# Kernel tuning notes

Hardware: AMD Instinct MI355X
Metric: run time of the kernel (lower is better)

The kernel has to match this reference:

```python
import jax, jax.numpy as jnp
import numpy as np

NB, NC = 100000, 10000   # buildings, communities
EB, EC = 400000, 80000   # edges
BD, CD = 64, 32          # feature dims


def _glorot(key, shape):
    fan_in = shape[-2] if len(shape) > 1 else shape[0]
    return jax.random.normal(key, shape, jnp.float32) * (1.0 / np.sqrt(fan_in))


def setup_inputs() -> dict:
    key = jax.random.key(0)
    ks = iter(jax.random.split(key, 40))
    inp = {}
    inp['building_features'] = jax.random.normal(next(ks), (NB, BD), jnp.float32)
    inp['community_features'] = jax.random.normal(next(ks), (NC, CD), jnp.float32)
    inp['building_edge_index'] = jax.random.randint(next(ks), (2, EB), 0, NB, jnp.int32)
    inp['community_edge_index'] = jax.random.randint(next(ks), (2, EC), 0, NC, jnp.int32)
    inp['building_to_comm_mapping'] = jax.random.randint(next(ks), (NB,), 0, NC, jnp.int32)
    inp['c1_wl'] = _glorot(next(ks), (CD, 512)); inp['c1_wr'] = _glorot(next(ks), (CD, 512))
    inp['c1_att'] = _glorot(next(ks), (8, 64)); inp['c1_b'] = jnp.zeros((512,), jnp.float32)
    inp['c2_wl'] = _glorot(next(ks), (512, 128)); inp['c2_wr'] = _glorot(next(ks), (512, 128))
    inp['c2_att'] = _glorot(next(ks), (4, 32)); inp['c2_b'] = jnp.zeros((128,), jnp.float32)
    # feature attention: 8 heads of MLP (64+128)->128->2
    inp['fa_w1'] = _glorot(next(ks), (8, BD + 128, 128)); inp['fa_b1'] = jnp.zeros((8, 128), jnp.float32)
    inp['fa_w2'] = _glorot(next(ks), (8, 128, 2)); inp['fa_b2'] = jnp.zeros((8, 2), jnp.float32)
    inp['b1_wl'] = _glorot(next(ks), (BD + 128, 512)); inp['b1_wr'] = _glorot(next(ks), (BD + 128, 512))
    inp['b1_att'] = _glorot(next(ks), (8, 64)); inp['b1_b'] = jnp.zeros((512,), jnp.float32)
    inp['b2_wl'] = _glorot(next(ks), (512, 128)); inp['b2_wr'] = _glorot(next(ks), (512, 128))
    inp['b2_att'] = _glorot(next(ks), (4, 32)); inp['b2_b'] = jnp.zeros((128,), jnp.float32)
    inp['b3_wl'] = _glorot(next(ks), (128, 2)); inp['b3_wr'] = _glorot(next(ks), (128, 2))
    inp['b3_att'] = _glorot(next(ks), (1, 2)); inp['b3_b'] = jnp.zeros((2,), jnp.float32)
    return inp


def gatv2(x, src, dst, wl, wr, att, b, heads, out_dim, concat=True):
    """PyG GATv2Conv (eval mode, self-loops already appended to src/dst)."""
    n = x.shape[0]
    xl = (x @ wl).reshape(n, heads, out_dim)  # source transform
    xr = (x @ wr).reshape(n, heads, out_dim)  # target transform
    e = jax.nn.leaky_relu(xl[src] + xr[dst], 0.2)          # [E,H,D]
    logits = jnp.einsum('ehd,hd->eh', e, att)              # [E,H]
    m = jax.ops.segment_max(logits, dst, num_segments=n)   # stable softmax per target
    p = jnp.exp(logits - m[dst])
    denom = jax.ops.segment_sum(p, dst, num_segments=n)
    alpha = p / denom[dst]
    agg = jax.ops.segment_sum(alpha[:, :, None] * xl[src], dst, num_segments=n)
    agg = agg.reshape(n, heads * out_dim) if concat else agg.mean(axis=1)
    return agg + b


def _with_self_loops(edge_index, n):
    loops = jnp.arange(n, dtype=edge_index.dtype)
    return (jnp.concatenate([edge_index[0], loops]), jnp.concatenate([edge_index[1], loops]))


def _forward(building_features, community_features,
             c1_wl, c1_wr, c1_att, c1_b, c2_wl, c2_wr, c2_att, c2_b,
             fa_w1, fa_b1, fa_w2, fa_b2,
             b1_wl, b1_wr, b1_att, b1_b, b2_wl, b2_wr, b2_att, b2_b,
             b3_wl, b3_wr, b3_att, b3_b,
             building_edge_index, community_edge_index, building_to_comm_mapping):
    csrc, cdst = _with_self_loops(community_edge_index, NC)
    bsrc, bdst = _with_self_loops(building_edge_index, NB)
    # community GNN (dropout is identity in eval)
    cx = jax.nn.relu(gatv2(community_features, csrc, cdst, c1_wl, c1_wr, c1_att, c1_b, 8, 64))
    cx = jax.nn.relu(gatv2(cx, csrc, cdst, c2_wl, c2_wr, c2_att, c2_b, 4, 32))  # [NC,128]
    bcf = cx[building_to_comm_mapping]                                          # [NB,128]
    # multi-head feature attention fusion (vectorized over 8 heads)
    combined = jnp.concatenate([building_features, bcf], axis=1)                # [NB,192]
    h = jax.nn.relu(jnp.einsum('nf,hfk->nhk', combined, fa_w1) + fa_b1)         # [NB,8,128]
    w = jax.nn.softmax(jnp.einsum('nhk,hko->nho', h, fa_w2) + fa_b2, axis=-1)   # [NB,8,2]
    wmean = w.mean(axis=1)                                                      # mean over heads == mean of weighted copies
    fused = jnp.concatenate([building_features * wmean[:, 0:1], bcf * wmean[:, 1:2]], axis=1)
    # building GNN (single batched graph == Batch.from_data_list over all communities)
    x = jax.nn.relu(gatv2(fused, bsrc, bdst, b1_wl, b1_wr, b1_att, b1_b, 8, 64))
    x = jax.nn.relu(gatv2(x, bsrc, bdst, b2_wl, b2_wr, b2_att, b2_b, 4, 32))
    x = gatv2(x, bsrc, bdst, b3_wl, b3_wr, b3_att, b3_b, 1, 2)                   # [NB,2]
    return jax.nn.log_softmax(x, axis=1)


def reference(building_features, community_features,
              c1_wl, c1_wr, c1_att, c1_b, c2_wl, c2_wr, c2_att, c2_b,
              fa_w1, fa_b1, fa_w2, fa_b2,
              b1_wl, b1_wr, b1_att, b1_b, b2_wl, b2_wr, b2_att, b2_b,
              b3_wl, b3_wr, b3_att, b3_b,
              building_edge_index, community_edge_index, building_to_comm_mapping):
    return _forward(building_features, community_features,
                    c1_wl, c1_wr, c1_att, c1_b, c2_wl, c2_wr, c2_att, c2_b,
                    fa_w1, fa_b1, fa_w2, fa_b2,
                    b1_wl, b1_wr, b1_att, b1_b, b2_wl, b2_wr, b2_att, b2_b,
                    b3_wl, b3_wr, b3_att, b3_b,
                    building_edge_index, community_edge_index, building_to_comm_mapping)
```

## Files before the change

### kernel.cpp

```cpp
#include <hip/hip_runtime.h>

static constexpr int NBLD = 100000, NCOM = 10000, EBU = 400000, ECO = 80000;
static constexpr int EBT = EBU + NBLD;
static constexpr int ECT = ECO + NCOM;

typedef _Float16 f16;
typedef _Float16 f16x2 __attribute__((ext_vector_type(2)));
typedef _Float16 f16x8 __attribute__((ext_vector_type(8)));
typedef float f32x4 __attribute__((ext_vector_type(4)));

static constexpr size_t OFF_X1H  = 0;
static constexpr size_t OFF_CXL  = 0;
static constexpr size_t OFF_CXR  = 20480000;
static constexpr size_t OFF_CX1  = 40960000;
static constexpr size_t OFF_CX2L = 61440000;
static constexpr size_t OFF_CX2R = 66560000;
static constexpr size_t OFF_X2   = 0;
static constexpr size_t OFF_XLH  = 102400000;
static constexpr size_t OFF_XRH  = 128000000;
static constexpr size_t OFF_XL2  = 102400000;
static constexpr size_t OFF_XR2  = 128000000;
static constexpr size_t OFF_BF16 = 153600000;
static constexpr size_t OFF_CXF16= 166400000;
static constexpr size_t OFF_WM   = 168960000;
static constexpr size_t OFF_XL3  = 169760000;
static constexpr size_t OFF_XR3  = 170560000;
static constexpr size_t OFF_FAW  = 171360000;
static constexpr size_t OFF_B1LT = 171753216;
static constexpr size_t OFF_B1RT = 171949824;
static constexpr size_t OFF_B2LT = 172146432;
static constexpr size_t OFF_B2RT = 172277504;
static constexpr size_t OFF_BOFF = 172408576;
static constexpr size_t OFF_BCUR = 172808592;
static constexpr size_t OFF_BSRC = 173208592;
static constexpr size_t OFF_COFF = 175208592;
static constexpr size_t OFF_CCUR = 175248608;
static constexpr size_t OFF_CSRC = 175288608;
static constexpr size_t OFF_SC1  = 175648608;
static constexpr size_t OFF_SC2  = 175649632;

__global__ void k_zero(int* __restrict__ p, int n) {
  int i = blockIdx.x * blockDim.x + threadIdx.x;
  if (i < n) p[i] = 0;
}

__global__ void k_zerof(float* __restrict__ p, int n) {
  int i = blockIdx.x * blockDim.x + threadIdx.x;
  if (i < n) p[i] = 0.f;
}

__global__ void k_cvt4(const float* __restrict__ a, f16* __restrict__ b, int n4) {
  int i = blockIdx.x * blockDim.x + threadIdx.x;
  if (i >= n4) return;
  float4 f = *(const float4*)(a + (size_t)i * 4);
  f16x2 h0; h0[0] = (f16)f.x; h0[1] = (f16)f.y;
  f16x2 h1; h1[0] = (f16)f.z; h1[1] = (f16)f.w;
  *(unsigned*)(b + (size_t)i * 4)     = __builtin_bit_cast(unsigned, h0);
  *(unsigned*)(b + (size_t)i * 4 + 2) = __builtin_bit_cast(unsigned, h1);
}

__global__ void k_cvtwb(const float* __restrict__ W, f16* __restrict__ WT, int K, int N) {
  int i = blockIdx.x * blockDim.x + threadIdx.x;
  if (i >= K * N) return;
  const float* Wb = W + (size_t)blockIdx.y * K * N;
  f16* Tb = WT + (size_t)blockIdx.y * K * N;
  int n = i / K, k = i - n * K;
  Tb[(size_t)n * K + k] = (f16)Wb[(size_t)k * N + n];
}

__global__ void k_count(const int* __restrict__ dsti, int Eg, int Et, int* __restrict__ cnt) {
  int e = blockIdx.x * blockDim.x + threadIdx.x;
  if (e >= Et) return;
  int dst = (e < Eg) ? dsti[e] : (e - Eg);
  atomicAdd(&cnt[dst], 1);
}

__global__ void k_scan1(const int* __restrict__ cnt, int N, int* __restrict__ off, int* __restrict__ bsum) {
  __shared__ int sh[256];
  int tid = threadIdx.x;
  int base = blockIdx.x * 2048 + tid * 8;
  int c[8]; int s = 0;
#pragma unroll
  for (int j = 0; j < 8; ++j) { int i = base + j; c[j] = (i < N) ? cnt[i] : 0; s += c[j]; }
  sh[tid] = s; __syncthreads();
  int own = s;
  for (int o = 1; o < 256; o <<= 1) {
    int v = (tid >= o) ? sh[tid - o] : 0; __syncthreads();
    sh[tid] += v; __syncthreads();
  }
  int ex = sh[tid] - own;
#pragma unroll
  for (int j = 0; j < 8; ++j) { int i = base + j; if (i < N) off[i] = ex; ex += c[j]; }
  if (tid == 255) bsum[blockIdx.x] = sh[255];
}

__global__ void k_scan2(const int* __restrict__ bsum, int nb, int* __restrict__ bpre) {
  __shared__ int sh[256];
  int tid = threadIdx.x;
  int v0 = (tid < nb) ? bsum[tid] : 0;
  sh[tid] = v0; __syncthreads();
  for (int o = 1; o < 256; o <<= 1) {
    int v = (tid >= o) ? sh[tid - o] : 0; __syncthreads();
    sh[tid] += v; __syncthreads();
  }
  bpre[tid] = sh[tid] - v0;
}

__global__ void k_scan3(int* __restrict__ off, int N, const int* __restrict__ bpre, int Et) {
  int i = blockIdx.x * blockDim.x + threadIdx.x;
  if (i < N) off[i] += bpre[i >> 11];
  if (i == 0) off[N] = Et;
}

__global__ void k_copycur(const int* __restrict__ off, int* __restrict__ cur, int N) {
  int i = blockIdx.x * blockDim.x + threadIdx.x;
  if (i < N) cur[i] = off[i];
}

__global__ void k_scatter(const int* __restrict__ srci, const int* __restrict__ dsti, int Eg, int Et,
                          int* __restrict__ cur, int* __restrict__ srcl) {
  int e = blockIdx.x * blockDim.x + threadIdx.x;
  if (e >= Et) return;
  int src, dst;
  if (e < Eg) { src = srci[e]; dst = dsti[e]; } else { src = dst = e - Eg; }
  int pos = atomicAdd(&cur[dst], 1);
  srcl[pos] = src;
}

template<bool ACCUM>
__global__ __launch_bounds__(256) void k_gemm_dual(
    const float* __restrict__ A,
    const float* __restrict__ W0, const float* __restrict__ W1,
    float* __restrict__ out0, float* __restrict__ out1,
    int M, int K, int lda, int ldw, int ldo) {
  __shared__ float As[16][132];
  __shared__ float Bs0[16][132];
  __shared__ float Bs1[16][132];
  int tid = threadIdx.x;
  int bm = blockIdx.y * 128, bn = blockIdx.x * 128;
  int tx = tid & 15, ty = tid >> 4;
  float acc0[8][8] = {{0.f}};
  float acc1[8][8] = {{0.f}};

  for (int k0 = 0; k0 < K; k0 += 16) {
    {
      int row = tid >> 1;
      int colh = (tid & 1) * 8;
      int gr = bm + row;
#pragma unroll
      for (int q = 0; q < 2; ++q) {
        int gc = k0 + colh + q * 4;
        float4 f = make_float4(0.f, 0.f, 0.f, 0.f);
        if (gr < M) f = *(const float4*)(A + (size_t)gr * lda + gc);
        int cb = colh + q * 4;
        As[cb + 0][row] = f.x; As[cb + 1][row] = f.y;
        As[cb + 2][row] = f.z; As[cb + 3][row] = f.w;
      }
    }
    {
      int r = tid >> 4;
      int c = (tid & 15) * 8;
#pragma unroll
      for (int q = 0; q < 2; ++q) {
        size_t wo = (size_t)(k0 + r) * ldw + bn + c + q * 4;
        *(float4*)&Bs0[r][c + q * 4] = *(const float4*)(W0 + wo);
        *(float4*)&Bs1[r][c + q * 4] = *(const float4*)(W1 + wo);
      }
    }
    __syncthreads();
#pragma unroll
    for (int kk = 0; kk < 16; ++kk) {
      float a[8], b0[8], b1[8];
#pragma unroll
      for (int i = 0; i < 8; ++i) a[i] = As[kk][ty * 8 + i];
#pragma unroll
      for (int j = 0; j < 8; ++j) b0[j] = Bs0[kk][tx * 8 + j];
#pragma unroll
      for (int j = 0; j < 8; ++j) b1[j] = Bs1[kk][tx * 8 + j];
#pragma unroll
      for (int i = 0; i < 8; ++i)
#pragma unroll
        for (int j = 0; j < 8; ++j) {
          acc0[i][j] = fmaf(a[i], b0[j], acc0[i][j]);
          acc1[i][j] = fmaf(a[i], b1[j], acc1[i][j]);
        }
    }
    __syncthreads();
  }
#pragma unroll
  for (int i = 0; i < 8; ++i) {
    int row = bm + ty * 8 + i;
    if (row >= M) continue;
#pragma unroll
    for (int j = 0; j < 8; j += 4) {
      int col = bn + tx * 8 + j;
      float4 v0 = make_float4(acc0[i][j], acc0[i][j + 1], acc0[i][j + 2], acc0[i][j + 3]);
      float4 v1 = make_float4(acc1[i][j], acc1[i][j + 1], acc1[i][j + 2], acc1[i][j + 3]);
      float4* p0 = (float4*)(out0 + (size_t)row * ldo + col);
      float4* p1 = (float4*)(out1 + (size_t)row * ldo + col);
      if (ACCUM) {
        float4 o0 = *p0, o1 = *p1;
        v0.x += o0.x; v0.y += o0.y; v0.z += o0.z; v0.w += o0.w;
        v1.x += o1.x; v1.y += o1.y; v1.z += o1.z; v1.w += o1.w;
      }
      *p0 = v0; *p1 = v1;
    }
  }
}


static __device__ inline void stage_BT(f16 (*Bs)[40], const f16* __restrict__ WT, int ldk,
                                       int k0, int tid) {
  int col = tid >> 1, half = tid & 1;
  const f16* p = WT + (size_t)col * ldk + k0 + half * 16;
  *(uint4*)&Bs[col][half * 16]     = *(const uint4*)(p);
  *(uint4*)&Bs[col][half * 16 + 8] = *(const uint4*)(p + 8);
}

static __device__ inline void stage_BTpair(f16 (*Bs)[40], const f16* __restrict__ WLt,
                                           const f16* __restrict__ WRt, int ldk, int slab,
                                           int k0, int tid) {
  int col = tid >> 1, half = tid & 1;
  const f16* base = (col < 64) ? (WLt + (size_t)(slab + col) * ldk)
                               : (WRt + (size_t)(slab + col - 64) * ldk);
  const f16* p = base + k0 + half * 16;
  *(uint4*)&Bs[col][half * 16]     = *(const uint4*)(p);
  *(uint4*)&Bs[col][half * 16 + 8] = *(const uint4*)(p + 8);
}

template<bool SCALE>
static __device__ inline void stage_A16(f16 (*As)[40], const f16* __restrict__ bf16h,
                                        const f16* __restrict__ cx16, int mrow,
                                        f16 s0, f16 s1, int k0, int tid, int grow, int M) {
  int row = tid >> 1, half = tid & 1;
  int gc = k0 + half * 16;
  f16x8 v0 = {}, v1 = {};
  if (grow < M) {
    const f16* src; f16 s;
    if (gc < 64) { src = bf16h + (size_t)grow * 64 + gc; s = s0; }
    else         { src = cx16 + (size_t)mrow * 128 + (gc - 64); s = s1; }
    v0 = *(const f16x8*)(src);
    v1 = *(const f16x8*)(src + 8);
    if (SCALE) {
#pragma unroll
      for (int j = 0; j < 8; ++j) { v0[j] *= s; v1[j] *= s; }
    }
  }
  *(f16x8*)&As[row][half * 16]     = v0;
  *(f16x8*)&As[row][half * 16 + 8] = v1;
}

static __device__ inline void stage_Ah(f16 (*As)[40], const f16* __restrict__ Xh, int lda,
                                       int k0, int tid, int bm, int M) {
  int row = tid >> 1;
  int half = tid & 1;
  int grow = bm + row;
  uint4 u0 = make_uint4(0, 0, 0, 0), u1 = make_uint4(0, 0, 0, 0);
  if (grow < M) {
    const f16* p = Xh + (size_t)grow * lda + k0 + half * 16;
    u0 = *(const uint4*)(p);
    u1 = *(const uint4*)(p + 8);
  }
  *(uint4*)&As[row][half * 16]     = u0;
  *(uint4*)&As[row][half * 16 + 8] = u1;
}

static __device__ inline void mma_tiles(const f16 (*As)[40], const f16 (*Bs)[40],
                                        f32x4 acc[4][4], int wm, int wn, int lane) {
  int rl = lane & 15;
  int kg = (lane >> 4) * 8;
  f16x8 a[4], b[4];
#pragma unroll
  for (int i = 0; i < 4; ++i) a[i] = *(const f16x8*)&As[wm * 64 + i * 16 + rl][kg];
#pragma unroll
  for (int j = 0; j < 4; ++j) b[j] = *(const f16x8*)&Bs[wn * 64 + j * 16 + rl][kg];
#pragma unroll
  for (int i = 0; i < 4; ++i)
#pragma unroll
    for (int j = 0; j < 4; ++j)
      acc[i][j] = __builtin_amdgcn_mfma_f32_16x16x32_f16(a[i], b[j], acc[i][j], 0, 0, 0);
}

__global__ __launch_bounds__(256) void k_mgemm_b1(
    const f16* __restrict__ bf16h, const f16* __restrict__ cx16,
    const int* __restrict__ map, const float* __restrict__ wmv,
    const f16* __restrict__ WLt, const f16* __restrict__ WRt, int slab,
    f16* __restrict__ outl, f16* __restrict__ outr, int colbase, int M) {
  __shared__ f16 As[128][40];
  __shared__ f16 Bs[128][40];
  int tid = threadIdx.x;
  int bm = blockIdx.x * 128;
  int lane = tid & 63, w = tid >> 6, wm_ = w >> 1, wn = w & 1;
  f32x4 acc[4][4];
#pragma unroll
  for (int i = 0; i < 4; ++i)
#pragma unroll
    for (int j = 0; j < 4; ++j) acc[i][j] = (f32x4){0.f, 0.f, 0.f, 0.f};

  int arow = bm + (tid >> 1);
  int mrow = 0; f16 s0 = (f16)1.f, s1 = (f16)1.f;
  if (arow < M) {
    mrow = map[arow];
    s0 = (f16)wmv[(size_t)arow * 2];
    s1 = (f16)wmv[(size_t)arow * 2 + 1];
  }

  for (int k0 = 0; k0 < 192; k0 += 32) {
    stage_A16<true>(As, bf16h, cx16, mrow, s0, s1, k0, tid, arow, M);
    stage_BTpair(Bs, WLt, WRt, 192, slab, k0, tid);
    __syncthreads();
    mma_tiles(As, Bs, acc, wm_, wn, lane);
    __syncthreads();
  }
  int rbase = bm + wm_ * 64 + (lane >> 4) * 4;
  int cl = lane & 15;
#pragma unroll
  for (int mi = 0; mi < 4; ++mi)
#pragma unroll
    for (int ni = 0; ni < 4; ++ni) {
      int col = wn * 64 + ni * 16 + cl;
      f16* o = (col < 64) ? outl : outr;
      int c = colbase + (col & 63);
#pragma unroll
      for (int r = 0; r < 4; ++r) {
        int row = rbase + mi * 16 + r;
        if (row < M) o[(size_t)row * 128 + c] = (f16)acc[mi][ni][r];
      }
    }
}

__global__ __launch_bounds__(256) void k_mgemm_b2(
    const f16* __restrict__ Xh,
    const f16* __restrict__ WlT, const f16* __restrict__ WrT,
    f16* __restrict__ outl, f16* __restrict__ outr, int M) {
  __shared__ f16 As[128][40];
  __shared__ f16 Bs[128][40];
  int tid = threadIdx.x;
  int bm = blockIdx.y * 128;
  const f16* WT = blockIdx.x ? WrT : WlT;
  f16* out = blockIdx.x ? outr : outl;
  int lane = tid & 63, w = tid >> 6, wm_ = w >> 1, wn = w & 1;
  f32x4 acc[4][4];
#pragma unroll
  for (int i = 0; i < 4; ++i)
#pragma unroll
    for (int j = 0; j < 4; ++j) acc[i][j] = (f32x4){0.f, 0.f, 0.f, 0.f};

  for (int k0 = 0; k0 < 512; k0 += 32) {
    stage_Ah(As, Xh, 512, k0, tid, bm, M);
    stage_BT(Bs, WT, 512, k0, tid);
    __syncthreads();
    mma_tiles(As, Bs, acc, wm_, wn, lane);
    __syncthreads();
  }
  int rbase = bm + wm_ * 64 + (lane >> 4) * 4;
  int cl = lane & 15;
#pragma unroll
  for (int mi = 0; mi < 4; ++mi)
#pragma unroll
    for (int ni = 0; ni < 4; ++ni) {
      int col = wn * 64 + ni * 16 + cl;
#pragma unroll
      for (int r = 0; r < 4; ++r) {
        int row = rbase + mi * 16 + r;
        if (row < M) out[(size_t)row * 128 + col] = (f16)acc[mi][ni][r];
      }
    }
}

__global__ __launch_bounds__(256) void k_mgemm_fa(
    const f16* __restrict__ bf16h, const f16* __restrict__ cx16,
    const int* __restrict__ map,
    const f16* __restrict__ w1T, const float* __restrict__ b1,
    const float* __restrict__ w2, const float* __restrict__ b2,
    float* __restrict__ wmout, int M) {
  __shared__ f16 As[128][40];
  __shared__ f16 Bs[128][40];
  __shared__ float sred[128][4];
  int tid = threadIdx.x;
  int ppx = gridDim.x >> 6;
  int xcd = blockIdx.x & 7;
  int j6 = blockIdx.x >> 3;
  int p = xcd * ppx + (j6 >> 3);
  int h = j6 & 7;
  int bm = p * 128;
  if (bm >= M) return;
  int lane = tid & 63, w = tid >> 6, wm_ = w >> 1, wn = w & 1;
  f32x4 acc[4][4];
#pragma unroll
  for (int i = 0; i < 4; ++i)
#pragma unroll
    for (int j = 0; j < 4; ++j) acc[i][j] = (f32x4){0.f, 0.f, 0.f, 0.f};

  int arow = bm + (tid >> 1);
  int mrow = (arow < M) ? map[arow] : 0;
  const f16* WT = w1T + (size_t)h * 128 * 192;

  for (int k0 = 0; k0 < 192; k0 += 32) {
    stage_A16<false>(As, bf16h, cx16, mrow, (f16)1.f, (f16)1.f, k0, tid, arow, M);
    stage_BT(Bs, WT, 192, k0, tid);
    __syncthreads();
    mma_tiles(As, Bs, acc, wm_, wn, lane);
    __syncthreads();
  }

  int cl = lane & 15;
#pragma unroll
  for (int mi = 0; mi < 4; ++mi) {
    float t0[4] = {0.f, 0.f, 0.f, 0.f}, t1[4] = {0.f, 0.f, 0.f, 0.f};
#pragma unroll
    for (int ni = 0; ni < 4; ++ni) {
      int col = wn * 64 + ni * 16 + cl;
      float b1c = b1[h * 128 + col];
      float w0c = w2[((size_t)h * 128 + col) * 2];
      float w1c = w2[((size_t)h * 128 + col) * 2 + 1];
#pragma unroll
      for (int r = 0; r < 4; ++r) {
        float hv = fmaxf(acc[mi][ni][r] + b1c, 0.f);
        t0[r] = fmaf(hv, w0c, t0[r]);
        t1[r] = fmaf(hv, w1c, t1[r]);
      }
    }
#pragma unroll
    for (int m = 1; m < 16; m <<= 1) {
#pragma unroll
      for (int r = 0; r < 4; ++r) { t0[r] += __shfl_xor(t0[r], m); t1[r] += __shfl_xor(t1[r], m); }
    }
    if (cl == 0) {
#pragma unroll
      for (int r = 0; r < 4; ++r) {
        int rib = wm_ * 64 + mi * 16 + (lane >> 4) * 4 + r;
        sred[rib][wn] = t0[r];
        sred[rib][2 + wn] = t1[r];
      }
    }
  }
  __syncthreads();
  if (tid < 128) {
    int grow = bm + tid;
    if (grow < M) {
      float l0 = sred[tid][0] + sred[tid][1] + b2[h * 2];
      float l1 = sred[tid][2] + sred[tid][3] + b2[h * 2 + 1];
      float mx = fmaxf(l0, l1);
      float e0 = __expf(l0 - mx), e1 = __expf(l1 - mx);
      float inv = 0.125f / (e0 + e1);
      atomicAdd(&wmout[(size_t)grow * 2], e0 * inv);
      atomicAdd(&wmout[(size_t)grow * 2 + 1], e1 * inv);
    }
  }
}

template<int V, int G, bool RELU, typename IT, typename OT>
__global__ __launch_bounds__(256) void k_convf(const IT* __restrict__ xl, const IT* __restrict__ xr,
                                               const float* __restrict__ attw, const float* __restrict__ bias,
                                               const int* __restrict__ off, const int* __restrict__ srcl,
                                               OT* __restrict__ outp, int N, int ldx, int ldo) {
  int n = (int)((blockIdx.x * (unsigned)blockDim.x + threadIdx.x) >> 6);
  if (n >= N) return;
  int lane = threadIdx.x & 63;
  int base = lane * V;
  float xr_r[V], att_r[V], acc[V];
#pragma unroll
  for (int j = 0; j < V; ++j) {
    xr_r[j] = (float)xr[(size_t)n * ldx + base + j];
    att_r[j] = attw[base + j];
    acc[j] = 0.f;
  }
  float mh = -INFINITY, lh = 0.f;
  int p0 = off[n], p1 = off[n + 1];
  for (int p = p0; p < p1; ++p) {
    int src = srcl[p];
    float xlv[V];
    if constexpr (V == 2 && sizeof(IT) == 2) {
      f16x2 t = *(const f16x2*)(&xl[(size_t)src * ldx + base]);
      xlv[0] = (float)t[0]; xlv[1] = (float)t[1];
    } else {
#pragma unroll
      for (int j = 0; j < V; ++j) xlv[j] = (float)xl[(size_t)src * ldx + base + j];
    }
    float part = 0.f;
#pragma unroll
    for (int j = 0; j < V; ++j) {
      float t = xlv[j] + xr_r[j];
      t = t > 0.f ? t : 0.2f * t;
      part = fmaf(t, att_r[j], part);
    }
#pragma unroll
    for (int m = 1; m < G; m <<= 1) part += __shfl_xor(part, m);
    float mn = fmaxf(mh, part);
    float scl = __expf(mh - mn);
    float pe = __expf(part - mn);
    lh = lh * scl + pe;
#pragma unroll
    for (int j = 0; j < V; ++j) acc[j] = acc[j] * scl + pe * xlv[j];
    mh = mn;
  }
  float inv = 1.f / lh;
#pragma unroll
  for (int j = 0; j < V; ++j) {
    float v = fmaf(acc[j], inv, bias[base + j]);
    if (RELU) v = fmaxf(v, 0.f);
    outp[(size_t)n * ldo + base + j] = (OT)v;
  }
}

__global__ __launch_bounds__(256) void k_b3gemm(const float* __restrict__ x2, const float* __restrict__ wl,
                                                const float* __restrict__ wr,
                                                float* __restrict__ xl3, float* __restrict__ xr3, int NB) {
  int n = (int)((blockIdx.x * (unsigned)blockDim.x + threadIdx.x) >> 6);
  if (n >= NB) return;
  int lane = threadIdx.x & 63;
  float2 a = *(const float2*)(x2 + (size_t)n * 128 + lane * 2);
  float4 wlv = *(const float4*)(wl + lane * 4);
  float4 wrv = *(const float4*)(wr + lane * 4);
  float l0 = a.x * wlv.x + a.y * wlv.z;
  float l1 = a.x * wlv.y + a.y * wlv.w;
  float r0 = a.x * wrv.x + a.y * wrv.z;
  float r1 = a.x * wrv.y + a.y * wrv.w;
#pragma unroll
  for (int m = 1; m < 64; m <<= 1) {
    l0 += __shfl_xor(l0, m); l1 += __shfl_xor(l1, m);
    r0 += __shfl_xor(r0, m); r1 += __shfl_xor(r1, m);
  }
  if (lane == 0) {
    xl3[(size_t)n * 2] = l0; xl3[(size_t)n * 2 + 1] = l1;
    xr3[(size_t)n * 2] = r0; xr3[(size_t)n * 2 + 1] = r1;
  }
}

__global__ void k_conv3(const float* __restrict__ xl, const float* __restrict__ xr,
                        const float* __restrict__ att, const float* __restrict__ bias,
                        const int* __restrict__ off, const int* __restrict__ srcl,
                        float* __restrict__ out, int NB) {
  int n = blockIdx.x * blockDim.x + threadIdx.x;
  if (n >= NB) return;
  float a0 = att[0], a1 = att[1];
  float xr0 = xr[(size_t)n * 2], xr1 = xr[(size_t)n * 2 + 1];
  float mh = -INFINITY, lh = 0.f, c0 = 0.f, c1 = 0.f;
  int p0 = off[n], p1 = off[n + 1];
  for (int p = p0; p < p1; ++p) {
    int src = srcl[p];
    float sl0 = xl[(size_t)src * 2], sl1 = xl[(size_t)src * 2 + 1];
    float t0 = sl0 + xr0; t0 = t0 > 0.f ? t0 : 0.2f * t0;
    float t1 = sl1 + xr1; t1 = t1 > 0.f ? t1 : 0.2f * t1;
    float lg = t0 * a0 + t1 * a1;
    float mn = fmaxf(mh, lg);
    float scl = __expf(mh - mn);
    float pe = __expf(lg - mn);
    lh = lh * scl + pe;
    c0 = c0 * scl + pe * sl0;
    c1 = c1 * scl + pe * sl1;
    mh = mn;
  }
  float inv = 1.f / lh;
  float v0 = c0 * inv + bias[0];
  float v1 = c1 * inv + bias[1];
  float mx = fmaxf(v0, v1);
  float ls = mx + logf(__expf(v0 - mx) + __expf(v1 - mx));
  out[(size_t)n * 2] = v0 - ls;
  out[(size_t)n * 2 + 1] = v1 - ls;
}

static inline int cdiv(int a, int b) { return (a + b - 1) / b; }

extern "C" void kernel_launch(void* const* d_in, const int* in_sizes, int n_in,
                              void* d_out, int out_size, void* d_ws, size_t ws_size,
                              hipStream_t stream) {
  (void)in_sizes; (void)n_in; (void)out_size; (void)ws_size;
  const float* bfeat = (const float*)d_in[0];
  const float* cfeat = (const float*)d_in[1];
  const int* bei = (const int*)d_in[2];
  const int* cei = (const int*)d_in[3];
  const int* b2c = (const int*)d_in[4];
  const float* c1_wl = (const float*)d_in[5];
  const float* c1_wr = (const float*)d_in[6];
  const float* c1_att = (const float*)d_in[7];
  const float* c1_b = (const float*)d_in[8];
  const float* c2_wl = (const float*)d_in[9];
  const float* c2_wr = (const float*)d_in[10];
  const float* c2_att = (const float*)d_in[11];
  const float* c2_b = (const float*)d_in[12];
  const float* fa_w1 = (const float*)d_in[13];
  const float* fa_b1 = (const float*)d_in[14];
  const float* fa_w2 = (const float*)d_in[15];
  const float* fa_b2 = (const float*)d_in[16];
  const float* b1_wl = (const float*)d_in[17];
  const float* b1_wr = (const float*)d_in[18];
  const float* b1_att = (const float*)d_in[19];
  const float* b1_b = (const float*)d_in[20];
  const float* b2_wl = (const float*)d_in[21];
  const float* b2_wr = (const float*)d_in[22];
  const float* b2_att = (const float*)d_in[23];
  const float* b2_b = (const float*)d_in[24];
  const float* b3_wl = (const float*)d_in[25];
  const float* b3_wr = (const float*)d_in[26];
  const float* b3_att = (const float*)d_in[27];
  const float* b3_b = (const float*)d_in[28];
  char* ws = (char*)d_ws;
  float* out = (float*)d_out;

  const int* b_src_arr = bei;
  const int* b_dst_arr = bei + EBU;
  const int* c_src_arr = cei;
  const int* c_dst_arr = cei + ECO;

  f16*   X1H  = (f16*)(ws + OFF_X1H);
  float* X2   = (float*)(ws + OFF_X2);
  f16*   XLH  = (f16*)(ws + OFF_XLH);
  f16*   XRH  = (f16*)(ws + OFF_XRH);
  f16*   XL2  = (f16*)(ws + OFF_XL2);
  f16*   XR2  = (f16*)(ws + OFF_XR2);
  float* CXL  = (float*)(ws + OFF_CXL);
  float* CXR  = (float*)(ws + OFF_CXR);
  float* CX1  = (float*)(ws + OFF_CX1);
  float* CX2L = (float*)(ws + OFF_CX2L);
  float* CX2R = (float*)(ws + OFF_CX2R);
  f16*   BF16 = (f16*)(ws + OFF_BF16);
  f16*   CXF16= (f16*)(ws + OFF_CXF16);
  float* WM   = (float*)(ws + OFF_WM);
  float* XL3  = (float*)(ws + OFF_XL3);
  float* XR3  = (float*)(ws + OFF_XR3);
  f16*   FAW  = (f16*)(ws + OFF_FAW);
  f16*   B1LT = (f16*)(ws + OFF_B1LT);
  f16*   B1RT = (f16*)(ws + OFF_B1RT);
  f16*   B2LT = (f16*)(ws + OFF_B2LT);
  f16*   B2RT = (f16*)(ws + OFF_B2RT);
  int* BOFF = (int*)(ws + OFF_BOFF);
  int* BCUR = (int*)(ws + OFF_BCUR);
  int* BSRC = (int*)(ws + OFF_BSRC);
  int* COFF = (int*)(ws + OFF_COFF);
  int* CCUR = (int*)(ws + OFF_CCUR);
  int* CSRC = (int*)(ws + OFF_CSRC);
  int* SC1  = (int*)(ws + OFF_SC1);
  int* SC2  = (int*)(ws + OFF_SC2);

  k_cvtwb<<<dim3(cdiv(192 * 128, 256), 8), 256, 0, stream>>>(fa_w1, FAW, 192, 128);
  k_cvtwb<<<dim3(cdiv(192 * 512, 256), 1), 256, 0, stream>>>(b1_wl, B1LT, 192, 512);
  k_cvtwb<<<dim3(cdiv(192 * 512, 256), 1), 256, 0, stream>>>(b1_wr, B1RT, 192, 512);
  k_cvtwb<<<dim3(cdiv(512 * 128, 256), 1), 256, 0, stream>>>(b2_wl, B2LT, 512, 128);
  k_cvtwb<<<dim3(cdiv(512 * 128, 256), 1), 256, 0, stream>>>(b2_wr, B2RT, 512, 128);
  k_cvt4<<<cdiv(NBLD * 16, 256), 256, 0, stream>>>(bfeat, BF16, NBLD * 16);

  k_zero<<<cdiv(NBLD, 256), 256, 0, stream>>>(BCUR, NBLD);
  k_count<<<cdiv(EBT, 256), 256, 0, stream>>>(b_dst_arr, EBU, EBT, BCUR);
  k_scan1<<<cdiv(NBLD, 2048), 256, 0, stream>>>(BCUR, NBLD, BOFF, SC1);
  k_scan2<<<1, 256, 0, stream>>>(SC1, cdiv(NBLD, 2048), SC2);
  k_scan3<<<cdiv(NBLD, 256), 256, 0, stream>>>(BOFF, NBLD, SC2, EBT);
  k_copycur<<<cdiv(NBLD, 256), 256, 0, stream>>>(BOFF, BCUR, NBLD);
  k_scatter<<<cdiv(EBT, 256), 256, 0, stream>>>(b_src_arr, b_dst_arr, EBU, EBT, BCUR, BSRC);
  k_zero<<<cdiv(NCOM, 256), 256, 0, stream>>>(CCUR, NCOM);
  k_count<<<cdiv(ECT, 256), 256, 0, stream>>>(c_dst_arr, ECO, ECT, CCUR);
  k_scan1<<<cdiv(NCOM, 2048), 256, 0, stream>>>(CCUR, NCOM, COFF, SC1);
  k_scan2<<<1, 256, 0, stream>>>(SC1, cdiv(NCOM, 2048), SC2);
  k_scan3<<<cdiv(NCOM, 256), 256, 0, stream>>>(COFF, NCOM, SC2, ECT);
  k_copycur<<<cdiv(NCOM, 256), 256, 0, stream>>>(COFF, CCUR, NCOM);
  k_scatter<<<cdiv(ECT, 256), 256, 0, stream>>>(c_src_arr, c_dst_arr, ECO, ECT, CCUR, CSRC);

  k_gemm_dual<false><<<dim3(4, cdiv(NCOM, 128)), 256, 0, stream>>>(
      cfeat, c1_wl, c1_wr, CXL, CXR, NCOM, 32, 32, 512, 512);
  k_convf<8, 8, true, float, float><<<cdiv(NCOM, 4), 256, 0, stream>>>(
      CXL, CXR, c1_att, c1_b, COFF, CSRC, CX1, NCOM, 512, 512);
  k_gemm_dual<false><<<dim3(1, cdiv(NCOM, 128)), 256, 0, stream>>>(
      CX1, c2_wl, c2_wr, CX2L, CX2R, NCOM, 512, 512, 128, 128);
  k_convf<2, 16, true, float, f16><<<cdiv(NCOM, 4), 256, 0, stream>>>(
      CX2L, CX2R, c2_att, c2_b, COFF, CSRC, CXF16, NCOM, 128, 128);

  k_zerof<<<cdiv(NBLD * 2, 256), 256, 0, stream>>>(WM, NBLD * 2);
  {
    int panels = cdiv(NBLD, 128);
    int ppx = cdiv(panels, 8);
    k_mgemm_fa<<<64 * ppx, 256, 0, stream>>>(
        BF16, CXF16, b2c, FAW, fa_b1, fa_w2, fa_b2, WM, NBLD);
  }

  for (int cp = 0; cp < 4; ++cp) {
    for (int ch = 0; ch < 2; ++ch) {
      int c = cp * 2 + ch;
      k_mgemm_b1<<<cdiv(NBLD, 128), 256, 0, stream>>>(
          BF16, CXF16, b2c, WM, B1LT, B1RT, c * 64, XLH, XRH, ch * 64, NBLD);
    }
    k_convf<2, 32, true, f16, f16><<<cdiv(NBLD, 4), 256, 0, stream>>>(
        XLH, XRH, b1_att + cp * 128, b1_b + cp * 128, BOFF, BSRC, X1H + cp * 128, NBLD, 128, 512);
  }

  k_mgemm_b2<<<dim3(2, cdiv(NBLD, 128)), 256, 0, stream>>>(
      X1H, B2LT, B2RT, XL2, XR2, NBLD);

  k_convf<2, 16, true, f16, float><<<cdiv(NBLD, 4), 256, 0, stream>>>(
      XL2, XR2, b2_att, b2_b, BOFF, BSRC, X2, NBLD, 128, 128);

  k_b3gemm<<<cdiv(NBLD, 4), 256, 0, stream>>>(X2, b3_wl, b3_wr, XL3, XR3, NBLD);
  k_conv3<<<cdiv(NBLD, 256), 256, 0, stream>>>(XL3, XR3, b3_att, b3_b, BOFF, BSRC, out, NBLD);
}
```

Baseline: 1.142 ms.

## Move community GEMMs to fp16 MFMA and merge b1/b2 GEMM launches with XCD-aware mapping

Replaces the fp32 SIMT dual GEMM for both community GATv2 layers with a generic fp16 MFMA GEMM, and stores the community intermediates in fp16 so the fp16 attention kernels read half the bytes. The two half-slab b1 GEMM launches per chunk become one launch, the b2 GEMM moves to the generic kernel with concatenated transposed weights, and block indices are remapped so that row panels are grouped per XCD. This adds conversion launches for the community features and weights, and lowers the precision of the community path.

```diff
diff --git a/kernel.cpp b/kernel.cpp
--- a/kernel.cpp
+++ b/kernel.cpp
@@ -11,10 +11,10 @@
 
 static constexpr size_t OFF_X1H  = 0;
 static constexpr size_t OFF_CXL  = 0;
-static constexpr size_t OFF_CXR  = 20480000;
-static constexpr size_t OFF_CX1  = 40960000;
-static constexpr size_t OFF_CX2L = 61440000;
-static constexpr size_t OFF_CX2R = 66560000;
+static constexpr size_t OFF_CXR  = 10240000;
+static constexpr size_t OFF_CX1  = 20480000;
+static constexpr size_t OFF_CX2L = 30720000;
+static constexpr size_t OFF_CX2R = 33280000;
 static constexpr size_t OFF_X2   = 0;
 static constexpr size_t OFF_XLH  = 102400000;
 static constexpr size_t OFF_XRH  = 128000000;
@@ -28,8 +28,7 @@
 static constexpr size_t OFF_FAW  = 171360000;
 static constexpr size_t OFF_B1LT = 171753216;
 static constexpr size_t OFF_B1RT = 171949824;
-static constexpr size_t OFF_B2LT = 172146432;
-static constexpr size_t OFF_B2RT = 172277504;
+static constexpr size_t OFF_B2T  = 172146432;
 static constexpr size_t OFF_BOFF = 172408576;
 static constexpr size_t OFF_BCUR = 172808592;
 static constexpr size_t OFF_BSRC = 173208592;
@@ -38,6 +37,9 @@
 static constexpr size_t OFF_CSRC = 175288608;
 static constexpr size_t OFF_SC1  = 175648608;
 static constexpr size_t OFF_SC2  = 175649632;
+static constexpr size_t OFF_C1T  = 175700000;
+static constexpr size_t OFF_C2T  = 175765536;
+static constexpr size_t OFF_CF16 = 176027680;
 
 __global__ void k_zero(int* __restrict__ p, int n) {
   int i = blockIdx.x * blockDim.x + threadIdx.x;
@@ -125,87 +127,6 @@
   if (e < Eg) { src = srci[e]; dst = dsti[e]; } else { src = dst = e - Eg; }
   int pos = atomicAdd(&cur[dst], 1);
   srcl[pos] = src;
-}
-
-template<bool ACCUM>
-__global__ __launch_bounds__(256) void k_gemm_dual(
-    const float* __restrict__ A,
-    const float* __restrict__ W0, const float* __restrict__ W1,
-    float* __restrict__ out0, float* __restrict__ out1,
-    int M, int K, int lda, int ldw, int ldo) {
-  __shared__ float As[16][132];
-  __shared__ float Bs0[16][132];
-  __shared__ float Bs1[16][132];
-  int tid = threadIdx.x;
-  int bm = blockIdx.y * 128, bn = blockIdx.x * 128;
-  int tx = tid & 15, ty = tid >> 4;
-  float acc0[8][8] = {{0.f}};
-  float acc1[8][8] = {{0.f}};
-
-  for (int k0 = 0; k0 < K; k0 += 16) {
-    {
-      int row = tid >> 1;
-      int colh = (tid & 1) * 8;
-      int gr = bm + row;
-#pragma unroll
-      for (int q = 0; q < 2; ++q) {
-        int gc = k0 + colh + q * 4;
-        float4 f = make_float4(0.f, 0.f, 0.f, 0.f);
-        if (gr < M) f = *(const float4*)(A + (size_t)gr * lda + gc);
-        int cb = colh + q * 4;
-        As[cb + 0][row] = f.x; As[cb + 1][row] = f.y;
-        As[cb + 2][row] = f.z; As[cb + 3][row] = f.w;
-      }
-    }
-    {
-      int r = tid >> 4;
-      int c = (tid & 15) * 8;
-#pragma unroll
-      for (int q = 0; q < 2; ++q) {
-        size_t wo = (size_t)(k0 + r) * ldw + bn + c + q * 4;
-        *(float4*)&Bs0[r][c + q * 4] = *(const float4*)(W0 + wo);
-        *(float4*)&Bs1[r][c + q * 4] = *(const float4*)(W1 + wo);
-      }
-    }
-    __syncthreads();
-#pragma unroll
-    for (int kk = 0; kk < 16; ++kk) {
-      float a[8], b0[8], b1[8];
-#pragma unroll
-      for (int i = 0; i < 8; ++i) a[i] = As[kk][ty * 8 + i];
-#pragma unroll
-      for (int j = 0; j < 8; ++j) b0[j] = Bs0[kk][tx * 8 + j];
-#pragma unroll
-      for (int j = 0; j < 8; ++j) b1[j] = Bs1[kk][tx * 8 + j];
-#pragma unroll
-      for (int i = 0; i < 8; ++i)
-#pragma unroll
-        for (int j = 0; j < 8; ++j) {
-          acc0[i][j] = fmaf(a[i], b0[j], acc0[i][j]);
-          acc1[i][j] = fmaf(a[i], b1[j], acc1[i][j]);
-        }
-    }
-    __syncthreads();
-  }
-#pragma unroll
-  for (int i = 0; i < 8; ++i) {
-    int row = bm + ty * 8 + i;
-    if (row >= M) continue;
-#pragma unroll
-    for (int j = 0; j < 8; j += 4) {
-      int col = bn + tx * 8 + j;
-      float4 v0 = make_float4(acc0[i][j], acc0[i][j + 1], acc0[i][j + 2], acc0[i][j + 3]);
-      float4 v1 = make_float4(acc1[i][j], acc1[i][j + 1], acc1[i][j + 2], acc1[i][j + 3]);
-      float4* p0 = (float4*)(out0 + (size_t)row * ldo + col);
-      float4* p1 = (float4*)(out1 + (size_t)row * ldo + col);
-      if (ACCUM) {
-        float4 o0 = *p0, o1 = *p1;
-        v0.x += o0.x; v0.y += o0.y; v0.z += o0.z; v0.w += o0.w;
-        v1.x += o1.x; v1.y += o1.y; v1.z += o1.z; v1.w += o1.w;
-      }
-      *p0 = v0; *p1 = v1;
-    }
-  }
 }
 
 
@@ -281,15 +202,71 @@
       acc[i][j] = __builtin_amdgcn_mfma_f32_16x16x32_f16(a[i], b[j], acc[i][j], 0, 0, 0);
 }
 
+template<int NCB>
+__global__ __launch_bounds__(256) void k_mgemm_gen(
+    const f16* __restrict__ A, int lda,
+    const f16* __restrict__ WT, int K,
+    f16* __restrict__ out0, f16* __restrict__ out1, int N0, int ldo, int M) {
+  __shared__ f16 As[128][40];
+  __shared__ f16 Bs[128][40];
+  int tid = threadIdx.x;
+  int ppx = gridDim.x / (8 * NCB);
+  int xcd = blockIdx.x & 7;
+  int j6 = blockIdx.x >> 3;
+  int cb = j6 % NCB;
+  int p = xcd * ppx + j6 / NCB;
+  int bm = p * 128;
+  if (bm >= M) return;
+  int bn = cb * 128;
+  int lane = tid & 63, w = tid >> 6, wm_ = w >> 1, wn = w & 1;
+  f32x4 acc[4][4];
+#pragma unroll
+  for (int i = 0; i < 4; ++i)
+#pragma unroll
+    for (int j = 0; j < 4; ++j) acc[i][j] = (f32x4){0.f, 0.f, 0.f, 0.f};
+
+  const f16* WTb = WT + (size_t)bn * K;
+  for (int k0 = 0; k0 < K; k0 += 32) {
+    stage_Ah(As, A, lda, k0, tid, bm, M);
+    stage_BT(Bs, WTb, K, k0, tid);
+    __syncthreads();
+    mma_tiles(As, Bs, acc, wm_, wn, lane);
+    __syncthreads();
+  }
+  int rbase = bm + wm_ * 64 + (lane >> 4) * 4;
+  int cl = lane & 15;
+#pragma unroll
+  for (int mi = 0; mi < 4; ++mi)
+#pragma unroll
+    for (int ni = 0; ni < 4; ++ni) {
+      int col = bn + wn * 64 + ni * 16 + cl;
+      f16* o; int c;
+      if (col < N0) { o = out0; c = col; } else { o = out1; c = col - N0; }
+#pragma unroll
+      for (int r = 0; r < 4; ++r) {
+        int row = rbase + mi * 16 + r;
+        if (row < M) o[(size_t)row * ldo + c] = (f16)acc[mi][ni][r];
+      }
+    }
+}
+
 __global__ __launch_bounds__(256) void k_mgemm_b1(
     const f16* __restrict__ bf16h, const f16* __restrict__ cx16,
     const int* __restrict__ map, const float* __restrict__ wmv,
-    const f16* __restrict__ WLt, const f16* __restrict__ WRt, int slab,
-    f16* __restrict__ outl, f16* __restrict__ outr, int colbase, int M) {
+    const f16* __restrict__ WLt, const f16* __restrict__ WRt, int slabBase,
+    f16* __restrict__ outl, f16* __restrict__ outr, int M) {
   __shared__ f16 As[128][40];
   __shared__ f16 Bs[128][40];
   int tid = threadIdx.x;
-  int bm = blockIdx.x * 128;
+  int ppx = gridDim.x >> 4;
+  int xcd = blockIdx.x & 7;
+  int j6 = blockIdx.x >> 3;
+  int ch = j6 & 1;
+  int p = xcd * ppx + (j6 >> 1);
+  int bm = p * 128;
+  if (bm >= M) return;
+  int slab = slabBase + ch * 64;
+  int colbase = ch * 64;
   int lane = tid & 63, w = tid >> 6, wm_ = w >> 1, wn = w & 1;
   f32x4 acc[4][4];
 #pragma unroll
@@ -325,45 +302,6 @@
       for (int r = 0; r < 4; ++r) {
         int row = rbase + mi * 16 + r;
         if (row < M) o[(size_t)row * 128 + c] = (f16)acc[mi][ni][r];
-      }
-    }
-}
-
-__global__ __launch_bounds__(256) void k_mgemm_b2(
-    const f16* __restrict__ Xh,
-    const f16* __restrict__ WlT, const f16* __restrict__ WrT,
-    f16* __restrict__ outl, f16* __restrict__ outr, int M) {
-  __shared__ f16 As[128][40];
-  __shared__ f16 Bs[128][40];
-  int tid = threadIdx.x;
-  int bm = blockIdx.y * 128;
-  const f16* WT = blockIdx.x ? WrT : WlT;
-  f16* out = blockIdx.x ? outr : outl;
-  int lane = tid & 63, w = tid >> 6, wm_ = w >> 1, wn = w & 1;
-  f32x4 acc[4][4];
-#pragma unroll
-  for (int i = 0; i < 4; ++i)
-#pragma unroll
-    for (int j = 0; j < 4; ++j) acc[i][j] = (f32x4){0.f, 0.f, 0.f, 0.f};
-
-  for (int k0 = 0; k0 < 512; k0 += 32) {
-    stage_Ah(As, Xh, 512, k0, tid, bm, M);
-    stage_BT(Bs, WT, 512, k0, tid);
-    __syncthreads();
-    mma_tiles(As, Bs, acc, wm_, wn, lane);
-    __syncthreads();
-  }
-  int rbase = bm + wm_ * 64 + (lane >> 4) * 4;
-  int cl = lane & 15;
-#pragma unroll
-  for (int mi = 0; mi < 4; ++mi)
-#pragma unroll
-    for (int ni = 0; ni < 4; ++ni) {
-      int col = wn * 64 + ni * 16 + cl;
-#pragma unroll
-      for (int r = 0; r < 4; ++r) {
-        int row = rbase + mi * 16 + r;
-        if (row < M) out[(size_t)row * 128 + col] = (f16)acc[mi][ni][r];
       }
     }
 }
@@ -474,6 +412,10 @@
     if constexpr (V == 2 && sizeof(IT) == 2) {
       f16x2 t = *(const f16x2*)(&xl[(size_t)src * ldx + base]);
       xlv[0] = (float)t[0]; xlv[1] = (float)t[1];
+    } else if constexpr (V == 8 && sizeof(IT) == 2) {
+      f16x8 t = *(const f16x8*)(&xl[(size_t)src * ldx + base]);
+#pragma unroll
+      for (int j = 0; j < 8; ++j) xlv[j] = (float)t[j];
     } else {
 #pragma unroll
       for (int j = 0; j < V; ++j) xlv[j] = (float)xl[(size_t)src * ldx + base + j];
@@ -610,11 +552,11 @@
   f16*   XRH  = (f16*)(ws + OFF_XRH);
   f16*   XL2  = (f16*)(ws + OFF_XL2);
   f16*   XR2  = (f16*)(ws + OFF_XR2);
-  float* CXL  = (float*)(ws + OFF_CXL);
-  float* CXR  = (float*)(ws + OFF_CXR);
-  float* CX1  = (float*)(ws + OFF_CX1);
-  float* CX2L = (float*)(ws + OFF_CX2L);
-  float* CX2R = (float*)(ws + OFF_CX2R);
+  f16*   CXLh = (f16*)(ws + OFF_CXL);
+  f16*   CXRh = (f16*)(ws + OFF_CXR);
+  f16*   CX1h = (f16*)(ws + OFF_CX1);
+  f16*   CX2Lh= (f16*)(ws + OFF_CX2L);
+  f16*   CX2Rh= (f16*)(ws + OFF_CX2R);
   f16*   BF16 = (f16*)(ws + OFF_BF16);
   f16*   CXF16= (f16*)(ws + OFF_CXF16);
   float* WM   = (float*)(ws + OFF_WM);
@@ -623,8 +565,10 @@
   f16*   FAW  = (f16*)(ws + OFF_FAW);
   f16*   B1LT = (f16*)(ws + OFF_B1LT);
   f16*   B1RT = (f16*)(ws + OFF_B1RT);
-  f16*   B2LT = (f16*)(ws + OFF_B2LT);
-  f16*   B2RT = (f16*)(ws + OFF_B2RT);
+  f16*   B2T  = (f16*)(ws + OFF_B2T);
+  f16*   C1T  = (f16*)(ws + OFF_C1T);
+  f16*   C2T  = (f16*)(ws + OFF_C2T);
+  f16*   CF16 = (f16*)(ws + OFF_CF16);
   int* BOFF = (int*)(ws + OFF_BOFF);
   int* BCUR = (int*)(ws + OFF_BCUR);
   int* BSRC = (int*)(ws + OFF_BSRC);
@@ -637,9 +581,14 @@
   k_cvtwb<<<dim3(cdiv(192 * 128, 256), 8), 256, 0, stream>>>(fa_w1, FAW, 192, 128);
   k_cvtwb<<<dim3(cdiv(192 * 512, 256), 1), 256, 0, stream>>>(b1_wl, B1LT, 192, 512);
   k_cvtwb<<<dim3(cdiv(192 * 512, 256), 1), 256, 0, stream>>>(b1_wr, B1RT, 192, 512);
-  k_cvtwb<<<dim3(cdiv(512 * 128, 256), 1), 256, 0, stream>>>(b2_wl, B2LT, 512, 128);
-  k_cvtwb<<<dim3(cdiv(512 * 128, 256), 1), 256, 0, stream>>>(b2_wr, B2RT, 512, 128);
+  k_cvtwb<<<dim3(cdiv(512 * 128, 256), 1), 256, 0, stream>>>(b2_wl, B2T, 512, 128);
+  k_cvtwb<<<dim3(cdiv(512 * 128, 256), 1), 256, 0, stream>>>(b2_wr, B2T + 128 * 512, 512, 128);
+  k_cvtwb<<<dim3(cdiv(32 * 512, 256), 1), 256, 0, stream>>>(c1_wl, C1T, 32, 512);
+  k_cvtwb<<<dim3(cdiv(32 * 512, 256), 1), 256, 0, stream>>>(c1_wr, C1T + 512 * 32, 32, 512);
+  k_cvtwb<<<dim3(cdiv(512 * 128, 256), 1), 256, 0, stream>>>(c2_wl, C2T, 512, 128);
+  k_cvtwb<<<dim3(cdiv(512 * 128, 256), 1), 256, 0, stream>>>(c2_wr, C2T + 128 * 512, 512, 128);
   k_cvt4<<<cdiv(NBLD * 16, 256), 256, 0, stream>>>(bfeat, BF16, NBLD * 16);
+  k_cvt4<<<cdiv(NCOM * 8, 256), 256, 0, stream>>>(cfeat, CF16, NCOM * 8);
 
   k_zero<<<cdiv(NBLD, 256), 256, 0, stream>>>(BCUR, NBLD);
   k_count<<<cdiv(EBT, 256), 256, 0, stream>>>(b_dst_arr, EBU, EBT, BCUR);
@@ -656,14 +605,17 @@
   k_copycur<<<cdiv(NCOM, 256), 256, 0, stream>>>(COFF, CCUR, NCOM);
   k_scatter<<<cdiv(ECT, 256), 256, 0, stream>>>(c_src_arr, c_dst_arr, ECO, ECT, CCUR, CSRC);
 
-  k_gemm_dual<false><<<dim3(4, cdiv(NCOM, 128)), 256, 0, stream>>>(
-      cfeat, c1_wl, c1_wr, CXL, CXR, NCOM, 32, 32, 512, 512);
-  k_convf<8, 8, true, float, float><<<cdiv(NCOM, 4), 256, 0, stream>>>(
-      CXL, CXR, c1_att, c1_b, COFF, CSRC, CX1, NCOM, 512, 512);
-  k_gemm_dual<false><<<dim3(1, cdiv(NCOM, 128)), 256, 0, stream>>>(
-      CX1, c2_wl, c2_wr, CX2L, CX2R, NCOM, 512, 512, 128, 128);
-  k_convf<2, 16, true, float, f16><<<cdiv(NCOM, 4), 256, 0, stream>>>(
-      CX2L, CX2R, c2_att, c2_b, COFF, CSRC, CXF16, NCOM, 128, 128);
+  {
+    int pC = cdiv(cdiv(NCOM, 128), 8);
+    k_mgemm_gen<8><<<8 * pC * 8, 256, 0, stream>>>(
+        CF16, 32, C1T, 32, CXLh, CXRh, 512, 512, NCOM);
+    k_convf<8, 8, true, f16, f16><<<cdiv(NCOM, 4), 256, 0, stream>>>(
+        CXLh, CXRh, c1_att, c1_b, COFF, CSRC, CX1h, NCOM, 512, 512);
+    k_mgemm_gen<2><<<8 * pC * 2, 256, 0, stream>>>(
+        CX1h, 512, C2T, 512, CX2Lh, CX2Rh, 128, 128, NCOM);
+    k_convf<2, 16, true, f16, f16><<<cdiv(NCOM, 4), 256, 0, stream>>>(
+        CX2Lh, CX2Rh, c2_att, c2_b, COFF, CSRC, CXF16, NCOM, 128, 128);
+  }
 
   k_zerof<<<cdiv(NBLD * 2, 256), 256, 0, stream>>>(WM, NBLD * 2);
   {
@@ -673,18 +625,17 @@
         BF16, CXF16, b2c, FAW, fa_b1, fa_w2, fa_b2, WM, NBLD);
   }
 
-  for (int cp = 0; cp < 4; ++cp) {
-    for (int ch = 0; ch < 2; ++ch) {
-      int c = cp * 2 + ch;
-      k_mgemm_b1<<<cdiv(NBLD, 128), 256, 0, stream>>>(
-          BF16, CXF16, b2c, WM, B1LT, B1RT, c * 64, XLH, XRH, ch * 64, NBLD);
-    }
-    k_convf<2, 32, true, f16, f16><<<cdiv(NBLD, 4), 256, 0, stream>>>(
-        XLH, XRH, b1_att + cp * 128, b1_b + cp * 128, BOFF, BSRC, X1H + cp * 128, NBLD, 128, 512);
-  }
-
-  k_mgemm_b2<<<dim3(2, cdiv(NBLD, 128)), 256, 0, stream>>>(
-      X1H, B2LT, B2RT, XL2, XR2, NBLD);
+  {
+    int pB = cdiv(cdiv(NBLD, 128), 8);
+    for (int cp = 0; cp < 4; ++cp) {
+      k_mgemm_b1<<<16 * pB, 256, 0, stream>>>(
+          BF16, CXF16, b2c, WM, B1LT, B1RT, cp * 128, XLH, XRH, NBLD);
+      k_convf<2, 32, true, f16, f16><<<cdiv(NBLD, 4), 256, 0, stream>>>(
+          XLH, XRH, b1_att + cp * 128, b1_b + cp * 128, BOFF, BSRC, X1H + cp * 128, NBLD, 128, 512);
+    }
+    k_mgemm_gen<2><<<8 * pB * 2, 256, 0, stream>>>(
+        X1H, 512, B2T, 512, XL2, XR2, 128, 128, NBLD);
+  }
 
   k_convf<2, 16, true, f16, float><<<cdiv(NBLD, 4), 256, 0, stream>>>(
       XL2, XR2, b2_att, b2_b, BOFF, BSRC, X2, NBLD, 128, 128);
```

Result: faster. 979.6 us (-14.2%).
